# Kernel optimization log

Measured on AMD Instinct MI355X. Metric: run time of the kernel, lower is better.

## Reference

```python
import jax, jax.numpy as jnp
import numpy as np

CUTOFFS = [16000, 28000, 36000]
HID = 1024
PROJ = [256, 64]  # hidden/4**1, hidden/4**2 per compute_proj_dims
CLUSTERS = 2


def setup_inputs() -> dict:
    key = jax.random.key(0)
    ks = jax.random.split(key, 12)
    B, S = 4, 1024
    scale = 0.02
    d = {
        "inp": jax.random.normal(ks[0], (B, S, HID), jnp.float32),
        "labels": jax.random.randint(ks[1], (B, S), 0, CUTOFFS[-1]),
        "head_W": jax.random.normal(ks[2], (HID, CUTOFFS[0] + CLUSTERS), jnp.float32) * scale,
        "head_b": jnp.zeros((CUTOFFS[0] + CLUSTERS,), jnp.float32),
    }
    for i in range(CLUSTERS):
        tdim = CUTOFFS[i + 1] - CUTOFFS[i]
        d[f"t{i}_pW"] = jax.random.normal(ks[3 + 4 * i], (HID, PROJ[i]), jnp.float32) * scale
        d[f"t{i}_pb"] = jnp.zeros((PROJ[i],), jnp.float32)
        d[f"t{i}_W"] = jax.random.normal(ks[4 + 4 * i], (PROJ[i], CUTOFFS[i + 1] - CUTOFFS[i]), jnp.float32) * scale
        d[f"t{i}_b"] = jnp.zeros((CUTOFFS[i + 1] - CUTOFFS[i],), jnp.float32)
    return d


def _sparse_ce(logits, labels):
    # stable sparse softmax cross entropy, single log_softmax pass
    logp = jax.nn.log_softmax(logits, axis=-1)
    return -jnp.take_along_axis(logp, labels[..., None], axis=-1)[..., 0]


def reference(inp, labels, head_W, head_b, t0_pW, t0_pb, t0_W, t0_b, t1_pW, t1_pb, t1_W, t1_b):
    tails = [(t0_pW, t0_pb, t0_W, t0_b), (t1_pW, t1_pb, t1_W, t1_b)]
    head_labels = labels
    loss = jnp.zeros(labels.shape, inp.dtype)
    for i, (pW, pb, W, b) in enumerate(tails):
        lo, hi = CUTOFFS[i], CUTOFFS[i + 1]
        mask = (labels >= lo) & (labels < hi)
        # tokens in cluster i are relabeled to cluster id in the head
        head_labels = jnp.where(mask, CUTOFFS[0] + i, head_labels)
        # two-layer tail projection: [B,S,H] -> [B,S,proj] -> [B,S,tail_dim]
        tail_logits = (inp @ pW + pb) @ W + b
        tail_labels = jnp.clip(labels - lo, 0, hi - lo - 1)
        loss = loss + jnp.where(mask, _sparse_ce(tail_logits, tail_labels), 0.0)
    head_logits = inp @ head_W + head_b  # [B,S,cutoffs[0]+clusters]
    loss = _sparse_ce(head_logits, head_labels) + loss
    loss = loss * (labels != 0).astype(loss.dtype)  # zero out pad positions
    return jnp.mean(loss)
```

## Files before the change

### kernel.cpp

```cpp
#include <hip/hip_runtime.h>
#include <hip/hip_bf16.h>
#include <hip/hip_fp8.h>
#include <cstdint>
#include <cstddef>

#define M_TOK 4096
#define HID   1024
#define NHEAD 16002
#define NHEAD_PAD 16128
#define P0    256
#define N0    12000
#define N0_PAD 12032
#define P1    64
#define N1    8000
#define N1_PAD 8192
#define PFUSE 384
#define PREAL 320

typedef unsigned char u8;
typedef float f32x4 __attribute__((ext_vector_type(4)));
typedef int   i32x4 __attribute__((ext_vector_type(4)));
typedef int   i32x8 __attribute__((ext_vector_type(8)));

__device__ __forceinline__ void load16(const void* g, void* l) {
    __builtin_amdgcn_global_load_lds(
        (__attribute__((address_space(1))) void*)g,
        (__attribute__((address_space(3))) void*)l,
        16, 0, 0);
}

__device__ __forceinline__ u8 to_e4m3(float f) {
    __hip_fp8_e4m3 h(f);
    return (u8)h.__x;
}

template <bool LSEP>
__device__ __forceinline__ void gemm_body(
        const u8* __restrict__ A, int lda, const u8* __restrict__ BT, int ldb,
        const float* __restrict__ bias, int K, int realN,
        const int* __restrict__ tgt, float* __restrict__ sumexp, float* __restrict__ lab,
        u8* __restrict__ out, int ldo, int m0, int n0,
        u8* As, u8* Bs) {
    const int tid  = threadIdx.x;
    const int lane = tid & 63;
    const int wave = tid >> 6;
    const int wm = wave >> 2, wn = wave & 3;
    const int q = lane >> 4, lrow = lane & 15;
    const int sw = lrow & 7;

    int aofs[2], bofs[2], lbase[2];
    #pragma unroll
    for (int p = 0; p < 2; p++) {
        int pg = wave * 128 + p * 64 + lane;
        int row = pg >> 3, gcol = (pg & 7) ^ (row & 7);
        aofs[p]  = row * lda + gcol * 16;
        bofs[p]  = row * ldb + gcol * 16;
        lbase[p] = (wave * 128 + p * 64) * 16;
    }

    f32x4 acc[4][2];
    #pragma unroll
    for (int mt = 0; mt < 4; mt++)
        #pragma unroll
        for (int nt = 0; nt < 2; nt++)
            acc[mt][nt] = (f32x4)(0.0f);

    const u8* Ab = A  + (size_t)m0 * lda;
    const u8* Bb = BT + (size_t)n0 * ldb;

    const int aLo = ((wm * 64 + lrow) * 8 + ((2 * q)     ^ sw)) * 16;
    const int aHi = ((wm * 64 + lrow) * 8 + ((2 * q + 1) ^ sw)) * 16;
    const int bLo = ((wn * 32 + lrow) * 8 + ((2 * q)     ^ sw)) * 16;
    const int bHi = ((wn * 32 + lrow) * 8 + ((2 * q + 1) ^ sw)) * 16;

    union Frag { struct { i32x4 lo, hi; } half; i32x8 v; };

    for (int k0 = 0; k0 < K; k0 += 128) {
        #pragma unroll
        for (int p = 0; p < 2; p++) {
            load16(Ab + k0 + aofs[p], As + lbase[p]);
            load16(Bb + k0 + bofs[p], Bs + lbase[p]);
        }
        __syncthreads();

        Frag fb[2];
        #pragma unroll
        for (int t = 0; t < 2; t++) {
            fb[t].half.lo = *reinterpret_cast<const i32x4*>(Bs + bLo + t * 2048);
            fb[t].half.hi = *reinterpret_cast<const i32x4*>(Bs + bHi + t * 2048);
        }
        #pragma unroll
        for (int mt = 0; mt < 4; mt++) {
            Frag fa;
            fa.half.lo = *reinterpret_cast<const i32x4*>(As + aLo + mt * 2048);
            fa.half.hi = *reinterpret_cast<const i32x4*>(As + aHi + mt * 2048);
            #pragma unroll
            for (int nt = 0; nt < 2; nt++)
                acc[mt][nt] = __builtin_amdgcn_mfma_scale_f32_16x16x128_f8f6f4(
                    fa.v, fb[nt].v, acc[mt][nt],
                    0, 0,
                    0, 0x7F7F7F7F,
                    0, 0x7A7A7A7A);
        }
        __syncthreads();
    }

    int colg[2]; float bias_v[2];
    #pragma unroll
    for (int nt = 0; nt < 2; nt++) {
        colg[nt] = n0 + wn * 32 + nt * 16 + lrow;
        bias_v[nt] = (colg[nt] < realN) ? bias[colg[nt]] : 0.0f;
    }

    float* sred = reinterpret_cast<float*>(As);

    #pragma unroll
    for (int mt = 0; mt < 4; mt++) {
        int rowb = m0 + wm * 64 + mt * 16 + q * 4;
        #pragma unroll
        for (int r = 0; r < 4; r++) {
            int tok = rowb + r;
            if constexpr (LSEP) {
                int tg = tgt[tok];
                float s = 0.0f;
                #pragma unroll
                for (int nt = 0; nt < 2; nt++) {
                    if (colg[nt] < realN) {
                        float logit = acc[mt][nt][r] + bias_v[nt];
                        s += __expf(logit);
                        if (colg[nt] == tg) atomicAdd(&lab[tok], logit);
                    }
                }
                s += __shfl_xor(s, 1);
                s += __shfl_xor(s, 2);
                s += __shfl_xor(s, 4);
                s += __shfl_xor(s, 8);
                if (lrow == 0) sred[wn * 128 + (wm * 64 + mt * 16 + q * 4 + r)] = s;
            } else {
                #pragma unroll
                for (int nt = 0; nt < 2; nt++)
                    out[(size_t)tok * ldo + colg[nt]] = to_e4m3(acc[mt][nt][r] + bias_v[nt]);
            }
        }
    }

    if constexpr (LSEP) {
        __syncthreads();
        if (tid < 128) {
            float v = sred[tid] + sred[128 + tid] + sred[256 + tid] + sred[384 + tid];
            atomicAdd(&sumexp[m0 + tid], v);
        }
    }
}

__launch_bounds__(512, 6)
__global__ void gemm_proj(const u8* __restrict__ A, const u8* __restrict__ BT,
                          const float* __restrict__ bias, u8* __restrict__ out) {
    __shared__ __align__(16) u8 As[16384];
    __shared__ __align__(16) u8 Bs[16384];
    gemm_body<false>(A, HID, BT, HID, bias, HID, PREAL,
                     nullptr, nullptr, nullptr, out, PFUSE,
                     blockIdx.x * 128, blockIdx.y * 128, As, Bs);
}

struct Seg {
    const u8* A; int lda;
    const u8* BT; int ldb;
    const float* bias; int K; int realN;
    const int* tgt; float* sumexp; float* lab;
    int nblk;
};

__launch_bounds__(512, 6)
__global__ void gemm_lse3(Seg s0, Seg s1, Seg s2) {
    __shared__ __align__(16) u8 As[16384];
    __shared__ __align__(16) u8 Bs[16384];
    int b = blockIdx.x;
    Seg s; int rel;
    if (b < s0.nblk)                { s = s0; rel = b; }
    else if (b < s0.nblk + s1.nblk) { s = s1; rel = b - s0.nblk; }
    else                            { s = s2; rel = b - s0.nblk - s1.nblk; }
    int pair = rel >> 6, inner = rel & 63;
    int m0 = (inner >> 1) * 128;
    int n0 = (pair * 2 + (inner & 1)) * 128;
    gemm_body<true>(s.A, s.lda, s.BT, s.ldb, s.bias, s.K, s.realN,
                    s.tgt, s.sumexp, s.lab, nullptr, 0, m0, n0, As, Bs);
}

__device__ __forceinline__ void do_transpose(const float* __restrict__ W, u8* __restrict__ WT,
                                             int K, int N, int Kpad, float scale,
                                             int bx, int by, float (*tile)[65]) {
    int n0 = bx * 64, k0 = by * 64;
    int c2 = threadIdx.x & 31;
    int rg = threadIdx.x >> 5;
    int n = n0 + c2 * 2;
    #pragma unroll
    for (int j = 0; j < 8; j++) {
        int k = k0 + rg + j * 8;
        float2 v;
        if (k < K && n + 1 < N) {
            v = *reinterpret_cast<const float2*>(&W[(size_t)k * N + n]);
        } else {
            v.x = (k < K && n     < N) ? W[(size_t)k * N + n]     : 0.0f;
            v.y = (k < K && n + 1 < N) ? W[(size_t)k * N + n + 1] : 0.0f;
        }
        tile[rg + j * 8][c2 * 2]     = v.x * scale;
        tile[rg + j * 8][c2 * 2 + 1] = v.y * scale;
    }
    __syncthreads();
    int nn = threadIdx.x >> 2, kb = (threadIdx.x & 3) * 16;
    union { u8 b[16]; uint4 u; } v;
    #pragma unroll
    for (int j = 0; j < 16; j++) v.b[j] = to_e4m3(tile[kb + j][nn]);
    *reinterpret_cast<uint4*>(WT + (size_t)(n0 + nn) * Kpad + k0 + kb) = v.u;
}

#define NBT_HEAD 4032
#define NBT_CAST 1024
#define NBT_T0W   752
#define NBT_T1W   256
#define NBT_T0P    64
#define NBT_T1P    32
#define NBT_INIT   16

__global__ void prep_kernel(const float* __restrict__ inp, const int* __restrict__ labels,
                            const float* __restrict__ head_W,
                            const float* __restrict__ t0_pW, const float* __restrict__ t0_pb,
                            const float* __restrict__ t0_W,
                            const float* __restrict__ t1_pW, const float* __restrict__ t1_pb,
                            const float* __restrict__ t1_W,
                            u8* __restrict__ inp_f8, u8* __restrict__ headW8,
                            u8* __restrict__ fpW8, u8* __restrict__ t0W8, u8* __restrict__ t1W8,
                            float* __restrict__ acc6, int* __restrict__ tgts,
                            float* __restrict__ pbias, float* __restrict__ out) {
    __shared__ float tile[64][65];
    int b = blockIdx.x;
    if (b < NBT_HEAD) {
        do_transpose(head_W, headW8, HID, NHEAD, HID, 32.0f, b % 252, b / 252, tile);
    } else if (b < NBT_HEAD + NBT_CAST) {
        int r = b - NBT_HEAD;
        int i = r * 256 + threadIdx.x;
        float4 v = reinterpret_cast<const float4*>(inp)[i];
        uchar4 o8;
        o8.x = to_e4m3(v.x); o8.y = to_e4m3(v.y); o8.z = to_e4m3(v.z); o8.w = to_e4m3(v.w);
        reinterpret_cast<uchar4*>(inp_f8)[i] = o8;
    } else if (b < NBT_HEAD + NBT_CAST + NBT_T0W) {
        int r = b - (NBT_HEAD + NBT_CAST);
        do_transpose(t0_W, t0W8, P0, N0, P0, 32.0f, r % 188, r / 188, tile);
    } else if (b < NBT_HEAD + NBT_CAST + NBT_T0W + NBT_T1W) {
        int r = b - (NBT_HEAD + NBT_CAST + NBT_T0W);
        do_transpose(t1_W, t1W8, P1, N1, 128, 32.0f, r % 128, r / 128, tile);
    } else if (b < NBT_HEAD + NBT_CAST + NBT_T0W + NBT_T1W + NBT_T0P) {
        int r = b - (NBT_HEAD + NBT_CAST + NBT_T0W + NBT_T1W);
        do_transpose(t0_pW, fpW8, HID, P0, HID, 32.0f, r % 4, r / 4, tile);
    } else if (b < NBT_HEAD + NBT_CAST + NBT_T0W + NBT_T1W + NBT_T0P + NBT_T1P) {
        int r = b - (NBT_HEAD + NBT_CAST + NBT_T0W + NBT_T1W + NBT_T0P);
        do_transpose(t1_pW, fpW8 + 256 * HID, HID, P1, HID, 32.0f, r % 2, r / 2, tile);
    } else {
        int r = b - (NBT_HEAD + NBT_CAST + NBT_T0W + NBT_T1W + NBT_T0P + NBT_T1P);
        int t = r * 256 + threadIdx.x;
        for (int j = t; j < 6 * M_TOK; j += M_TOK) acc6[j] = 0.0f;
        if (t == 0) out[0] = 0.0f;
        if (t < PFUSE) pbias[t] = (t < 256) ? t0_pb[t] : ((t < PREAL) ? t1_pb[t - 256] : 0.0f);
        int lbl = labels[t];
        tgts[t]             = (lbl < 16000) ? lbl : ((lbl < 28000) ? 16000 : 16001);
        int t0 = lbl - 16000; t0 = t0 < 0 ? 0 : (t0 > 11999 ? 11999 : t0);
        int t1 = lbl - 28000; t1 = t1 < 0 ? 0 : (t1 > 7999  ? 7999  : t1);
        tgts[M_TOK + t]     = t0;
        tgts[2 * M_TOK + t] = t1;
    }
}

__global__ void finalize_kernel(const int* __restrict__ labels, const float* __restrict__ acc6,
                                float* __restrict__ out) {
    int t = blockIdx.x * blockDim.x + threadIdx.x;
    const float* sumH = acc6;
    const float* labH = acc6 + M_TOK;
    const float* sum0 = acc6 + 2 * M_TOK;
    const float* lab0 = acc6 + 3 * M_TOK;
    const float* sum1 = acc6 + 4 * M_TOK;
    const float* lab1 = acc6 + 5 * M_TOK;
    int lbl = labels[t];
    float l = 0.0f;
    if (lbl != 0) {
        l = logf(sumH[t]) - labH[t];
        if (lbl >= 16000 && lbl < 28000) l += logf(sum0[t]) - lab0[t];
        else if (lbl >= 28000)           l += logf(sum1[t]) - lab1[t];
    }
    l *= (1.0f / (float)M_TOK);
    #pragma unroll
    for (int off = 1; off < 64; off <<= 1) l += __shfl_xor(l, off);
    __shared__ float red[4];
    if ((threadIdx.x & 63) == 0) red[threadIdx.x >> 6] = l;
    __syncthreads();
    if (threadIdx.x == 0) atomicAdd(out, red[0] + red[1] + red[2] + red[3]);
}

extern "C" void kernel_launch(void* const* d_in, const int* in_sizes, int n_in,
                              void* d_out, int out_size, void* d_ws, size_t ws_size,
                              hipStream_t stream) {
    const float* inp    = (const float*)d_in[0];
    const int*   labels = (const int*)  d_in[1];
    const float* head_W = (const float*)d_in[2];
    const float* head_b = (const float*)d_in[3];
    const float* t0_pW  = (const float*)d_in[4];
    const float* t0_pb  = (const float*)d_in[5];
    const float* t0_W   = (const float*)d_in[6];
    const float* t0_b   = (const float*)d_in[7];
    const float* t1_pW  = (const float*)d_in[8];
    const float* t1_pb  = (const float*)d_in[9];
    const float* t1_W   = (const float*)d_in[10];
    const float* t1_b   = (const float*)d_in[11];
    float* out = (float*)d_out;

    char* ws = (char*)d_ws;
    size_t off = 0;
    auto alloc = [&](size_t bytes) { char* p = ws + off; off += (bytes + 255) & ~(size_t)255; return p; };
    u8*    inp_f8  = (u8*)   alloc((size_t)M_TOK * HID);
    u8*    headW8  = (u8*)   alloc((size_t)NHEAD_PAD * HID);
    u8*    fpW8    = (u8*)   alloc((size_t)PFUSE * HID);
    u8*    t0W8    = (u8*)   alloc((size_t)N0_PAD * P0);
    u8*    t1W8    = (u8*)   alloc((size_t)N1_PAD * 128);
    u8*    proj8   = (u8*)   alloc((size_t)M_TOK * PFUSE);
    float* acc6    = (float*)alloc(6 * M_TOK * 4);
    int*   tgts    = (int*)  alloc(3 * M_TOK * 4);
    float* pbias   = (float*)alloc(PFUSE * 4);

    int nb = NBT_HEAD + NBT_CAST + NBT_T0W + NBT_T1W + NBT_T0P + NBT_T1P + NBT_INIT;
    prep_kernel<<<nb, 256, 0, stream>>>(inp, labels, head_W, t0_pW, t0_pb, t0_W,
                                        t1_pW, t1_pb, t1_W,
                                        inp_f8, headW8, fpW8, t0W8, t1W8,
                                        acc6, tgts, pbias, out);

    gemm_proj<<<dim3(M_TOK / 128, PFUSE / 128), 512, 0, stream>>>(inp_f8, fpW8, pbias, proj8);

    Seg s0{inp_f8,      HID,   headW8, HID, head_b, HID, NHEAD, tgts,             acc6,             acc6 + M_TOK,     32 * (NHEAD_PAD / 128)};
    Seg s1{proj8,       PFUSE, t0W8,   P0,  t0_b,   P0,  N0,    tgts + M_TOK,     acc6 + 2 * M_TOK, acc6 + 3 * M_TOK, 32 * (N0_PAD / 128)};
    Seg s2{proj8 + 256, PFUSE, t1W8,   128, t1_b,   128, N1,    tgts + 2 * M_TOK, acc6 + 4 * M_TOK, acc6 + 5 * M_TOK, 32 * (N1_PAD / 128)};
    gemm_lse3<<<s0.nblk + s1.nblk + s2.nblk, 512, 0, stream>>>(s0, s1, s2);

    finalize_kernel<<<M_TOK / 256, 256, 0, stream>>>(labels, acc6, out);
}
```

Before: 331.4 us.

## Enlarge LSE GEMM tiles to 256x256 with double-buffered LDS pipeline

Raises the fused head/tail logsumexp GEMM from 128x128 tiles with 512 threads to 256x256 tiles with 1024 threads. Each wave now computes a 64x64 sub-tile. Global-to-LDS loads are double-buffered with explicit vmcnt waits and barriers so the next K-slice loads while the current one computes. Vocab padding grows to multiples of 256, which adds some wasted columns. The kernel uses 128KB of LDS and 1024 threads per block, which lowers occupancy and risks register pressure from the larger accumulator set.

```diff
diff --git a/kernel.cpp b/kernel.cpp
--- a/kernel.cpp
+++ b/kernel.cpp
@@ -7,10 +7,10 @@
 #define M_TOK 4096
 #define HID   1024
 #define NHEAD 16002
-#define NHEAD_PAD 16128
+#define NHEAD_PAD 16384
 #define P0    256
 #define N0    12000
-#define N0_PAD 12032
+#define N0_PAD 12288
 #define P1    64
 #define N1    8000
 #define N1_PAD 8192
@@ -34,13 +34,31 @@
     return (u8)h.__x;
 }
 
-template <bool LSEP>
-__device__ __forceinline__ void gemm_body(
-        const u8* __restrict__ A, int lda, const u8* __restrict__ BT, int ldb,
-        const float* __restrict__ bias, int K, int realN,
-        const int* __restrict__ tgt, float* __restrict__ sumexp, float* __restrict__ lab,
-        u8* __restrict__ out, int ldo, int m0, int n0,
-        u8* As, u8* Bs) {
+union Frag { struct { i32x4 lo, hi; } half; i32x8 v; };
+
+struct Seg {
+    const u8* A; int lda;
+    const u8* BT; int ldb;
+    const float* bias; int K; int realN;
+    const int* tgt; float* sumexp; float* lab;
+    int nblk;
+};
+
+__launch_bounds__(1024, 4)
+__global__ void gemm_lse3(Seg s0, Seg s1, Seg s2) {
+    __shared__ __align__(16) u8 As[2 * 32768];
+    __shared__ __align__(16) u8 Bs[2 * 32768];
+
+    int b = blockIdx.x;
+    Seg sg; int rel;
+    if (b < s0.nblk)                { sg = s0; rel = b; }
+    else if (b < s0.nblk + s1.nblk) { sg = s1; rel = b - s0.nblk; }
+    else                            { sg = s2; rel = b - s0.nblk - s1.nblk; }
+    int pair = rel >> 5, inner = rel & 31;
+    int m0 = (inner >> 1) * 256;
+    int n0 = (pair * 2 + (inner & 1)) * 256;
+
+    const int lda = sg.lda, ldb = sg.ldb;
     const int tid  = threadIdx.x;
     const int lane = tid & 63;
     const int wave = tid >> 6;
@@ -58,6 +76,136 @@
         lbase[p] = (wave * 128 + p * 64) * 16;
     }
 
+    f32x4 acc[4][4];
+    #pragma unroll
+    for (int mt = 0; mt < 4; mt++)
+        #pragma unroll
+        for (int nt = 0; nt < 4; nt++)
+            acc[mt][nt] = (f32x4)(0.0f);
+
+    const u8* Ab = sg.A  + (size_t)m0 * lda;
+    const u8* Bb = sg.BT + (size_t)n0 * ldb;
+
+    const int aLo = ((wm * 64 + lrow) * 8 + ((2 * q)     ^ sw)) * 16;
+    const int aHi = ((wm * 64 + lrow) * 8 + ((2 * q + 1) ^ sw)) * 16;
+    const int bLo = ((wn * 64 + lrow) * 8 + ((2 * q)     ^ sw)) * 16;
+    const int bHi = ((wn * 64 + lrow) * 8 + ((2 * q + 1) ^ sw)) * 16;
+
+    auto stage = [&](int buf, int k0) {
+        #pragma unroll
+        for (int p = 0; p < 2; p++) {
+            load16(Ab + k0 + aofs[p], As + buf * 32768 + lbase[p]);
+            load16(Bb + k0 + bofs[p], Bs + buf * 32768 + lbase[p]);
+        }
+    };
+
+    auto compute = [&](int buf) {
+        const u8* Ac = As + buf * 32768;
+        const u8* Bc = Bs + buf * 32768;
+        Frag fb[4];
+        #pragma unroll
+        for (int t = 0; t < 4; t++) {
+            fb[t].half.lo = *reinterpret_cast<const i32x4*>(Bc + bLo + t * 2048);
+            fb[t].half.hi = *reinterpret_cast<const i32x4*>(Bc + bHi + t * 2048);
+        }
+        Frag fa[2];
+        fa[0].half.lo = *reinterpret_cast<const i32x4*>(Ac + aLo);
+        fa[0].half.hi = *reinterpret_cast<const i32x4*>(Ac + aHi);
+        #pragma unroll
+        for (int mt = 0; mt < 4; mt++) {
+            if (mt < 3) {
+                fa[(mt + 1) & 1].half.lo = *reinterpret_cast<const i32x4*>(Ac + aLo + (mt + 1) * 2048);
+                fa[(mt + 1) & 1].half.hi = *reinterpret_cast<const i32x4*>(Ac + aHi + (mt + 1) * 2048);
+            }
+            #pragma unroll
+            for (int nt = 0; nt < 4; nt++)
+                acc[mt][nt] = __builtin_amdgcn_mfma_scale_f32_16x16x128_f8f6f4(
+                    fa[mt & 1].v, fb[nt].v, acc[mt][nt],
+                    0, 0,
+                    0, 0x7F7F7F7F,
+                    0, 0x7A7A7A7A);
+        }
+    };
+
+    const int ntile = sg.K >> 7;
+    stage(0, 0);
+    for (int t = 0; t < ntile; ++t) {
+        int cur = t & 1;
+        if (t + 1 < ntile) {
+            stage(cur ^ 1, (t + 1) << 7);
+            asm volatile("s_waitcnt vmcnt(4)" ::: "memory");
+        } else {
+            asm volatile("s_waitcnt vmcnt(0)" ::: "memory");
+        }
+        asm volatile("s_barrier" ::: "memory");
+        compute(cur);
+        asm volatile("s_waitcnt lgkmcnt(0)" ::: "memory");
+        asm volatile("s_barrier" ::: "memory");
+    }
+
+    int colg[4]; float bias_v[4];
+    #pragma unroll
+    for (int nt = 0; nt < 4; nt++) {
+        colg[nt] = n0 + wn * 64 + nt * 16 + lrow;
+        bias_v[nt] = (colg[nt] < sg.realN) ? sg.bias[colg[nt]] : 0.0f;
+    }
+
+    float* sred = reinterpret_cast<float*>(As);
+
+    #pragma unroll
+    for (int mt = 0; mt < 4; mt++) {
+        int rloc = wm * 64 + mt * 16 + q * 4;
+        #pragma unroll
+        for (int r = 0; r < 4; r++) {
+            int tok = m0 + rloc + r;
+            int tg = sg.tgt[tok];
+            float ps = 0.0f;
+            #pragma unroll
+            for (int nt = 0; nt < 4; nt++) {
+                if (colg[nt] < sg.realN) {
+                    float logit = acc[mt][nt][r] + bias_v[nt];
+                    ps += __expf(logit);
+                    if (colg[nt] == tg) atomicAdd(&sg.lab[tok], logit);
+                }
+            }
+            ps += __shfl_xor(ps, 1);
+            ps += __shfl_xor(ps, 2);
+            ps += __shfl_xor(ps, 4);
+            ps += __shfl_xor(ps, 8);
+            if (lrow == 0) sred[wn * 256 + rloc + r] = ps;
+        }
+    }
+    __syncthreads();
+    if (tid < 256) {
+        float v = sred[tid] + sred[256 + tid] + sred[512 + tid] + sred[768 + tid];
+        atomicAdd(&sg.sumexp[m0 + tid], v);
+    }
+}
+
+__launch_bounds__(512, 6)
+__global__ void gemm_proj(const u8* __restrict__ A, const u8* __restrict__ BT,
+                          const float* __restrict__ bias, u8* __restrict__ out) {
+    __shared__ __align__(16) u8 As[16384];
+    __shared__ __align__(16) u8 Bs[16384];
+    const int lda = HID, ldb = HID, ldo = PFUSE;
+    const int m0 = blockIdx.x * 128, n0 = blockIdx.y * 128;
+    const int tid  = threadIdx.x;
+    const int lane = tid & 63;
+    const int wave = tid >> 6;
+    const int wm = wave >> 2, wn = wave & 3;
+    const int q = lane >> 4, lrow = lane & 15;
+    const int sw = lrow & 7;
+
+    int aofs[2], bofs[2], lbase[2];
+    #pragma unroll
+    for (int p = 0; p < 2; p++) {
+        int pg = wave * 128 + p * 64 + lane;
+        int row = pg >> 3, gcol = (pg & 7) ^ (row & 7);
+        aofs[p]  = row * lda + gcol * 16;
+        bofs[p]  = row * ldb + gcol * 16;
+        lbase[p] = (wave * 128 + p * 64) * 16;
+    }
+
     f32x4 acc[4][2];
     #pragma unroll
     for (int mt = 0; mt < 4; mt++)
@@ -73,16 +221,13 @@
     const int bLo = ((wn * 32 + lrow) * 8 + ((2 * q)     ^ sw)) * 16;
     const int bHi = ((wn * 32 + lrow) * 8 + ((2 * q + 1) ^ sw)) * 16;
 
-    union Frag { struct { i32x4 lo, hi; } half; i32x8 v; };
-
-    for (int k0 = 0; k0 < K; k0 += 128) {
+    for (int k0 = 0; k0 < HID; k0 += 128) {
         #pragma unroll
         for (int p = 0; p < 2; p++) {
             load16(Ab + k0 + aofs[p], As + lbase[p]);
             load16(Bb + k0 + bofs[p], Bs + lbase[p]);
         }
         __syncthreads();
-
         Frag fb[2];
         #pragma unroll
         for (int t = 0; t < 2; t++) {
@@ -98,9 +243,7 @@
             for (int nt = 0; nt < 2; nt++)
                 acc[mt][nt] = __builtin_amdgcn_mfma_scale_f32_16x16x128_f8f6f4(
                     fa.v, fb[nt].v, acc[mt][nt],
-                    0, 0,
-                    0, 0x7F7F7F7F,
-                    0, 0x7A7A7A7A);
+                    0, 0, 0, 0x7F7F7F7F, 0, 0x7A7A7A7A);
         }
         __syncthreads();
     }
@@ -109,82 +252,19 @@
     #pragma unroll
     for (int nt = 0; nt < 2; nt++) {
         colg[nt] = n0 + wn * 32 + nt * 16 + lrow;
-        bias_v[nt] = (colg[nt] < realN) ? bias[colg[nt]] : 0.0f;
-    }
-
-    float* sred = reinterpret_cast<float*>(As);
-
+        bias_v[nt] = (colg[nt] < PREAL) ? bias[colg[nt]] : 0.0f;
+    }
     #pragma unroll
     for (int mt = 0; mt < 4; mt++) {
         int rowb = m0 + wm * 64 + mt * 16 + q * 4;
         #pragma unroll
         for (int r = 0; r < 4; r++) {
             int tok = rowb + r;
-            if constexpr (LSEP) {
-                int tg = tgt[tok];
-                float s = 0.0f;
-                #pragma unroll
-                for (int nt = 0; nt < 2; nt++) {
-                    if (colg[nt] < realN) {
-                        float logit = acc[mt][nt][r] + bias_v[nt];
-                        s += __expf(logit);
-                        if (colg[nt] == tg) atomicAdd(&lab[tok], logit);
-                    }
-                }
-                s += __shfl_xor(s, 1);
-                s += __shfl_xor(s, 2);
-                s += __shfl_xor(s, 4);
-                s += __shfl_xor(s, 8);
-                if (lrow == 0) sred[wn * 128 + (wm * 64 + mt * 16 + q * 4 + r)] = s;
-            } else {
-                #pragma unroll
-                for (int nt = 0; nt < 2; nt++)
-                    out[(size_t)tok * ldo + colg[nt]] = to_e4m3(acc[mt][nt][r] + bias_v[nt]);
-            }
-        }
-    }
-
-    if constexpr (LSEP) {
-        __syncthreads();
-        if (tid < 128) {
-            float v = sred[tid] + sred[128 + tid] + sred[256 + tid] + sred[384 + tid];
-            atomicAdd(&sumexp[m0 + tid], v);
-        }
-    }
-}
-
-__launch_bounds__(512, 6)
-__global__ void gemm_proj(const u8* __restrict__ A, const u8* __restrict__ BT,
-                          const float* __restrict__ bias, u8* __restrict__ out) {
-    __shared__ __align__(16) u8 As[16384];
-    __shared__ __align__(16) u8 Bs[16384];
-    gemm_body<false>(A, HID, BT, HID, bias, HID, PREAL,
-                     nullptr, nullptr, nullptr, out, PFUSE,
-                     blockIdx.x * 128, blockIdx.y * 128, As, Bs);
-}
-
-struct Seg {
-    const u8* A; int lda;
-    const u8* BT; int ldb;
-    const float* bias; int K; int realN;
-    const int* tgt; float* sumexp; float* lab;
-    int nblk;
-};
-
-__launch_bounds__(512, 6)
-__global__ void gemm_lse3(Seg s0, Seg s1, Seg s2) {
-    __shared__ __align__(16) u8 As[16384];
-    __shared__ __align__(16) u8 Bs[16384];
-    int b = blockIdx.x;
-    Seg s; int rel;
-    if (b < s0.nblk)                { s = s0; rel = b; }
-    else if (b < s0.nblk + s1.nblk) { s = s1; rel = b - s0.nblk; }
-    else                            { s = s2; rel = b - s0.nblk - s1.nblk; }
-    int pair = rel >> 6, inner = rel & 63;
-    int m0 = (inner >> 1) * 128;
-    int n0 = (pair * 2 + (inner & 1)) * 128;
-    gemm_body<true>(s.A, s.lda, s.BT, s.ldb, s.bias, s.K, s.realN,
-                    s.tgt, s.sumexp, s.lab, nullptr, 0, m0, n0, As, Bs);
+            #pragma unroll
+            for (int nt = 0; nt < 2; nt++)
+                out[(size_t)tok * ldo + colg[nt]] = to_e4m3(acc[mt][nt][r] + bias_v[nt]);
+        }
+    }
 }
 
 __device__ __forceinline__ void do_transpose(const float* __restrict__ W, u8* __restrict__ WT,
@@ -215,9 +295,9 @@
     *reinterpret_cast<uint4*>(WT + (size_t)(n0 + nn) * Kpad + k0 + kb) = v.u;
 }
 
-#define NBT_HEAD 4032
+#define NBT_HEAD 4096
 #define NBT_CAST 1024
-#define NBT_T0W   752
+#define NBT_T0W   768
 #define NBT_T1W   256
 #define NBT_T0P    64
 #define NBT_T1P    32
@@ -236,7 +316,7 @@
     __shared__ float tile[64][65];
     int b = blockIdx.x;
     if (b < NBT_HEAD) {
-        do_transpose(head_W, headW8, HID, NHEAD, HID, 32.0f, b % 252, b / 252, tile);
+        do_transpose(head_W, headW8, HID, NHEAD, HID, 32.0f, b % 256, b / 256, tile);
     } else if (b < NBT_HEAD + NBT_CAST) {
         int r = b - NBT_HEAD;
         int i = r * 256 + threadIdx.x;
@@ -246,7 +326,7 @@
         reinterpret_cast<uchar4*>(inp_f8)[i] = o8;
     } else if (b < NBT_HEAD + NBT_CAST + NBT_T0W) {
         int r = b - (NBT_HEAD + NBT_CAST);
-        do_transpose(t0_W, t0W8, P0, N0, P0, 32.0f, r % 188, r / 188, tile);
+        do_transpose(t0_W, t0W8, P0, N0, P0, 32.0f, r % 192, r / 192, tile);
     } else if (b < NBT_HEAD + NBT_CAST + NBT_T0W + NBT_T1W) {
         int r = b - (NBT_HEAD + NBT_CAST + NBT_T0W);
         do_transpose(t1_W, t1W8, P1, N1, 128, 32.0f, r % 128, r / 128, tile);
@@ -334,10 +414,10 @@
 
     gemm_proj<<<dim3(M_TOK / 128, PFUSE / 128), 512, 0, stream>>>(inp_f8, fpW8, pbias, proj8);
 
-    Seg s0{inp_f8,      HID,   headW8, HID, head_b, HID, NHEAD, tgts,             acc6,             acc6 + M_TOK,     32 * (NHEAD_PAD / 128)};
-    Seg s1{proj8,       PFUSE, t0W8,   P0,  t0_b,   P0,  N0,    tgts + M_TOK,     acc6 + 2 * M_TOK, acc6 + 3 * M_TOK, 32 * (N0_PAD / 128)};
-    Seg s2{proj8 + 256, PFUSE, t1W8,   128, t1_b,   128, N1,    tgts + 2 * M_TOK, acc6 + 4 * M_TOK, acc6 + 5 * M_TOK, 32 * (N1_PAD / 128)};
-    gemm_lse3<<<s0.nblk + s1.nblk + s2.nblk, 512, 0, stream>>>(s0, s1, s2);
+    Seg s0{inp_f8,      HID,   headW8, HID, head_b, HID, NHEAD, tgts,             acc6,             acc6 + M_TOK,     16 * (NHEAD_PAD / 256)};
+    Seg s1{proj8,       PFUSE, t0W8,   P0,  t0_b,   P0,  N0,    tgts + M_TOK,     acc6 + 2 * M_TOK, acc6 + 3 * M_TOK, 16 * (N0_PAD / 256)};
+    Seg s2{proj8 + 256, PFUSE, t1W8,   128, t1_b,   128, N1,    tgts + 2 * M_TOK, acc6 + 4 * M_TOK, acc6 + 5 * M_TOK, 16 * (N1_PAD / 256)};
+    gemm_lse3<<<s0.nblk + s1.nblk + s2.nblk, 1024, 0, stream>>>(s0, s1, s2);
 
     finalize_kernel<<<M_TOK / 256, 256, 0, stream>>>(labels, acc6, out);
 }
```

New measurement: 309.6 us. 1.07x faster.
